# Kernel tuning notes

Hardware: AMD Instinct MI355X
Metric: run time of the kernel (lower is better)

## Reference

```python
import jax, jax.numpy as jnp
import numpy as np

K = 31  # box-filter kernel size
PAD = 15

def _avg_pool_31(x):
    # count_include_pad=True (torch default): divide by K*K everywhere
    s = jax.lax.reduce_window(x, 0.0, jax.lax.add,
                              window_dimensions=(1, 1, K, K),
                              window_strides=(1, 1, 1, 1),
                              padding=((0, 0), (0, 0), (PAD, PAD), (PAD, PAD)))
    return s / (K * K)

def setup_inputs() -> dict:
    key = jax.random.key(0)
    k1, k2 = jax.random.split(key)
    pred = jax.random.normal(k1, (64, 1, 512, 512), dtype=jnp.float32)
    mask = jax.random.uniform(k2, (64, 1, 512, 512), dtype=jnp.float32)
    return {"pred": pred, "mask": mask}

def reference(pred, mask):
    weight = 1.0 + 5.0 * jnp.abs(_avg_pool_31(mask) - mask)
    # binary_cross_entropy_with_logits, reduction='none' (stable form)
    bce = jnp.maximum(pred, 0.0) - pred * mask + jnp.log1p(jnp.exp(-jnp.abs(pred)))
    p = jax.nn.sigmoid(pred)
    inter = p * mask
    union = p + mask
    iou = 1.0 - (inter + 1.0) / (union - inter + 1.0)
    wsum = weight.sum(axis=(2, 3))  # [B, C]
    weighted_bce = (weight * bce).sum(axis=(2, 3)) / wsum
    weighted_iou = (weight * iou).sum(axis=(2, 3)) / wsum
    return (weighted_bce + weighted_iou).mean()
```

## Files before the change

kernel.cpp:

```cpp
#include <hip/hip_runtime.h>
#include <math.h>

#define BATCH 64
#define H 512
#define W 512
#define KRAD 15
#define STRIP 64
#define NSTRIP (H / STRIP)
#define RING 48

__device__ __forceinline__ float wave_reduce(float v) {
    #pragma unroll
    for (int off = 32; off > 0; off >>= 1) v += __shfl_xor(v, off);
    return v;
}

__device__ __forceinline__ unsigned bf16b(float f) {
    unsigned u = __float_as_uint(f);
    return (u + 0x7FFFu + ((u >> 16) & 1u)) >> 16;
}
__device__ __forceinline__ float fbf16(unsigned short s) {
    return __uint_as_float(((unsigned)s) << 16);
}

__device__ __forceinline__ void scan_row(const float* __restrict__ img_base, int r,
                                         int lane, unsigned short* dst) {
    float o[8];
    if (0 <= r && r < H) {
        const float4* in4 = reinterpret_cast<const float4*>(img_base + (size_t)r * W + lane * 8);
        float4 va = in4[0], vb = in4[1];
        float v[8] = {va.x, va.y, va.z, va.w, vb.x, vb.y, vb.z, vb.w};
        float P[8];
        P[0] = v[0];
        #pragma unroll
        for (int k = 1; k < 8; ++k) P[k] = P[k - 1] + v[k];
        const float T = P[7];

        float Tm1 = __shfl_up(T, 1);
        float Tm2 = __shfl_up(T, 2);
        float Tp1 = __shfl_down(T, 1);
        float Pm2[7], Pp2[7];
        #pragma unroll
        for (int k = 0; k < 7; ++k) Pm2[k] = __shfl_up(P[k], 2);
        #pragma unroll
        for (int k = 0; k < 7; ++k) Pp2[k] = __shfl_down(P[k], 2);

        if (lane < 1) Tm1 = 0.f;
        if (lane < 2) {
            Tm2 = 0.f;
            #pragma unroll
            for (int k = 0; k < 7; ++k) Pm2[k] = 0.f;
        }
        if (lane > 62) Tp1 = 0.f;
        if (lane > 61) {
            #pragma unroll
            for (int k = 0; k < 7; ++k) Pp2[k] = 0.f;
        }

        const float C = Tm1 + T + Tp1;
        o[0] = C + (Tm2 - Pm2[0]);
        #pragma unroll
        for (int k = 1; k < 7; ++k) o[k] = C + (Tm2 - Pm2[k]) + Pp2[k - 1];
        o[7] = C + Pp2[6];
    } else {
        #pragma unroll
        for (int k = 0; k < 8; ++k) o[k] = 0.f;
    }
    uint4 wv;
    wv.x = bf16b(o[0]) | (bf16b(o[1]) << 16);
    wv.y = bf16b(o[2]) | (bf16b(o[3]) << 16);
    wv.z = bf16b(o[4]) | (bf16b(o[5]) << 16);
    wv.w = bf16b(o[6]) | (bf16b(o[7]) << 16);
    *reinterpret_cast<uint4*>(dst + lane * 8) = wv;
}

__global__ __launch_bounds__(512) void fused_kernel(const float* __restrict__ pred,
                                                    const float* __restrict__ mask,
                                                    float2* __restrict__ partials) {
    __shared__ unsigned short ring[RING][W];

    const int tid  = threadIdx.x;
    const int wave = tid >> 6;
    const int lane = tid & 63;
    const int img   = blockIdx.x >> 3;
    const int strip = blockIdx.x & 7;
    const int r0 = strip * STRIP;
    const int c  = tid;
    const float* mk = mask + (size_t)img * (H * W);
    const float* pr = pred + (size_t)img * (H * W);

    #pragma unroll
    for (int gp = 0; gp < 4; ++gp) {
        const int idx = gp * 8 + wave;
        if (idx < 31) scan_row(mk, r0 - 16 + idx, lane, &ring[idx][0]);
    }
    __syncthreads();

    float vsum = 0.f;
    #pragma unroll
    for (int s = 1; s <= 30; ++s) vsum += fbf16(ring[s][c]);

    float s0 = 0.f, s1 = 0.f;
    const float inv_k2 = 1.0f / 961.0f;
    int sA = 31;
    int sB = 0;

    for (int g = 0; g < STRIP / 8; ++g) {
        const int ybase = r0 + 8 * g;
        {
            int slot = sA + wave;
            if (slot >= RING) slot -= RING;
            scan_row(mk, ybase + 15 + wave, lane, &ring[slot][0]);
        }
        __syncthreads();

        float m[8], p[8];
        #pragma unroll
        for (int i = 0; i < 8; ++i) {
            const int y = ybase + i;
            m[i] = mk[(size_t)y * W + c];
            p[i] = pr[(size_t)y * W + c];
        }
        float addv[8], subv[8];
        #pragma unroll
        for (int i = 0; i < 8; ++i) {
            int slotA = sA + i;
            if (slotA >= RING) slotA -= RING;
            addv[i] = fbf16(ring[slotA][c]);
            subv[i] = fbf16(ring[sB + i][c]);
        }
        float ws[8];
        {
            float acc = vsum;
            #pragma unroll
            for (int i = 0; i < 8; ++i) { acc += addv[i] - subv[i]; ws[i] = acc; }
            vsum = acc;
        }
        #pragma unroll
        for (int i = 0; i < 8; ++i) {
            const float avg = ws[i] * inv_k2;
            const float w = 1.0f + 5.0f * fabsf(avg - m[i]);

            const float e = __expf(-fabsf(p[i]));
            const float u = 1.0f + e;
            const float softplus = __logf(u);
            const float bce = fmaxf(p[i], 0.0f) - p[i] * m[i] + softplus;

            const float a = (p[i] >= 0.0f) ? 1.0f : e;
            const float num = a * m[i] + u;
            const float den = a * (1.0f - m[i]) + (m[i] + 1.0f) * u;
            const float iou = 1.0f - num * __builtin_amdgcn_rcpf(den);

            s0 += w;
            s1 += w * (bce + iou);
        }
        sA += 8; if (sA >= RING) sA -= RING;
        sB += 8; if (sB >= RING) sB -= RING;
    }

    s0 = wave_reduce(s0);
    s1 = wave_reduce(s1);
    __syncthreads();
    float2* wacc = reinterpret_cast<float2*>(&ring[0][0]);
    if (lane == 0) wacc[wave] = make_float2(s0, s1);
    __syncthreads();
    if (tid == 0) {
        float a0 = 0.f, a1 = 0.f;
        #pragma unroll
        for (int i = 0; i < 8; ++i) { a0 += wacc[i].x; a1 += wacc[i].y; }
        partials[blockIdx.x] = make_float2(a0, a1);
    }
}

__global__ void finalize_kernel(const float2* __restrict__ partials,
                                float* __restrict__ out) {
    const int lane = threadIdx.x;
    float s0 = 0.f, s1 = 0.f;
    #pragma unroll
    for (int j = 0; j < NSTRIP; ++j) {
        const float2 pp = partials[lane * NSTRIP + j];
        s0 += pp.x; s1 += pp.y;
    }
    float q = s1 / s0;
    q = wave_reduce(q);
    if (lane == 0) out[0] = q * (1.0f / (float)BATCH);
}

extern "C" void kernel_launch(void* const* d_in, const int* in_sizes, int n_in,
                              void* d_out, int out_size, void* d_ws, size_t ws_size,
                              hipStream_t stream) {
    const float* pred = (const float*)d_in[0];
    const float* mask = (const float*)d_in[1];
    float2* partials = (float2*)d_ws;

    hipLaunchKernelGGL(fused_kernel, dim3(BATCH * NSTRIP), dim3(512), 0, stream,
                       pred, mask, partials);
    hipLaunchKernelGGL(finalize_kernel, dim3(1), dim3(64), 0, stream,
                       partials, (float*)d_out);
}
```

Before: 41.94 us.

## Double block size, split rows between two thread halves with stride-2 sliding window

Blocks now have 1024 threads, and the two 512-thread halves process even and odd output rows of each 16-row group. Each half advances its vertical running sum by two rows per step, adding two new ring rows and subtracting two old ones. The ring grows to 64 rows with power-of-two masking, and the horizontal-scan prologue uses 16 waves. The aim is more parallelism per strip, with the number of barriers per strip halved, at the cost of extra LDS reads per output row and a larger shared allocation (64 KB) that may cut blocks per CU.

New measurement: 55.00 us. +31.2%, slower.

```diff
diff --git a/kernel.cpp b/kernel.cpp
--- a/kernel.cpp
+++ b/kernel.cpp
@@ -7,7 +7,8 @@
 #define KRAD 15
 #define STRIP 64
 #define NSTRIP (H / STRIP)
-#define RING 48
+#define GROUP 16
+#define RING 64
 
 __device__ __forceinline__ float wave_reduce(float v) {
     #pragma unroll
@@ -74,9 +75,9 @@
     *reinterpret_cast<uint4*>(dst + lane * 8) = wv;
 }
 
-__global__ __launch_bounds__(512) void fused_kernel(const float* __restrict__ pred,
-                                                    const float* __restrict__ mask,
-                                                    float2* __restrict__ partials) {
+__global__ __launch_bounds__(1024) void fused_kernel(const float* __restrict__ pred,
+                                                     const float* __restrict__ mask,
+                                                     float2* __restrict__ partials) {
     __shared__ unsigned short ring[RING][W];
 
     const int tid  = threadIdx.x;
@@ -85,60 +86,47 @@
     const int img   = blockIdx.x >> 3;
     const int strip = blockIdx.x & 7;
     const int r0 = strip * STRIP;
-    const int c  = tid;
+    const int c    = tid & 511;
+    const int half = tid >> 9;
     const float* mk = mask + (size_t)img * (H * W);
     const float* pr = pred + (size_t)img * (H * W);
 
     #pragma unroll
-    for (int gp = 0; gp < 4; ++gp) {
-        const int idx = gp * 8 + wave;
-        if (idx < 31) scan_row(mk, r0 - 16 + idx, lane, &ring[idx][0]);
+    for (int pass = 0; pass < 2; ++pass) {
+        const int idx2 = pass * 16 + wave;
+        scan_row(mk, r0 - 17 + idx2, lane, &ring[(idx2 + 63) & 63][0]);
     }
     __syncthreads();
 
     float vsum = 0.f;
     #pragma unroll
-    for (int s = 1; s <= 30; ++s) vsum += fbf16(ring[s][c]);
+    for (int s = 0; s <= 30; ++s) vsum += fbf16(ring[(half + s + 63) & 63][c]);
 
     float s0 = 0.f, s1 = 0.f;
     const float inv_k2 = 1.0f / 961.0f;
-    int sA = 31;
-    int sB = 0;
 
-    for (int g = 0; g < STRIP / 8; ++g) {
-        const int ybase = r0 + 8 * g;
-        {
-            int slot = sA + wave;
-            if (slot >= RING) slot -= RING;
-            scan_row(mk, ybase + 15 + wave, lane, &ring[slot][0]);
-        }
+    for (int g = 0; g < STRIP / GROUP; ++g) {
+        const int ob = 16 * g;
+        scan_row(mk, r0 + ob + 15 + wave, lane, &ring[(ob + 31 + wave) & 63][0]);
         __syncthreads();
 
         float m[8], p[8];
         #pragma unroll
         for (int i = 0; i < 8; ++i) {
-            const int y = ybase + i;
+            const int y = r0 + ob + 2 * i + half;
             m[i] = mk[(size_t)y * W + c];
             p[i] = pr[(size_t)y * W + c];
         }
-        float addv[8], subv[8];
         #pragma unroll
         for (int i = 0; i < 8; ++i) {
-            int slotA = sA + i;
-            if (slotA >= RING) slotA -= RING;
-            addv[i] = fbf16(ring[slotA][c]);
-            subv[i] = fbf16(ring[sB + i][c]);
-        }
-        float ws[8];
-        {
-            float acc = vsum;
-            #pragma unroll
-            for (int i = 0; i < 8; ++i) { acc += addv[i] - subv[i]; ws[i] = acc; }
-            vsum = acc;
-        }
-        #pragma unroll
-        for (int i = 0; i < 8; ++i) {
-            const float avg = ws[i] * inv_k2;
+            const int o = ob + 2 * i + half;
+            const float a1 = fbf16(ring[(o + 31) & 63][c]);
+            const float a2 = fbf16(ring[(o + 30) & 63][c]);
+            const float b1 = fbf16(ring[(o     ) & 63][c]);
+            const float b2 = fbf16(ring[(o + 63) & 63][c]);
+            vsum += (a1 + a2) - (b1 + b2);
+
+            const float avg = vsum * inv_k2;
             const float w = 1.0f + 5.0f * fabsf(avg - m[i]);
 
             const float e = __expf(-fabsf(p[i]));
@@ -154,8 +142,6 @@
             s0 += w;
             s1 += w * (bce + iou);
         }
-        sA += 8; if (sA >= RING) sA -= RING;
-        sB += 8; if (sB >= RING) sB -= RING;
     }
 
     s0 = wave_reduce(s0);
@@ -167,7 +153,7 @@
     if (tid == 0) {
         float a0 = 0.f, a1 = 0.f;
         #pragma unroll
-        for (int i = 0; i < 8; ++i) { a0 += wacc[i].x; a1 += wacc[i].y; }
+        for (int i = 0; i < 16; ++i) { a0 += wacc[i].x; a1 += wacc[i].y; }
         partials[blockIdx.x] = make_float2(a0, a1);
     }
 }
@@ -193,7 +179,7 @@
     const float* mask = (const float*)d_in[1];
     float2* partials = (float2*)d_ws;
 
-    hipLaunchKernelGGL(fused_kernel, dim3(BATCH * NSTRIP), dim3(512), 0, stream,
+    hipLaunchKernelGGL(fused_kernel, dim3(BATCH * NSTRIP), dim3(1024), 0, stream,
                        pred, mask, partials);
     hipLaunchKernelGGL(finalize_kernel, dim3(1), dim3(64), 0, stream,
                        partials, (float*)d_out);
```
